# Kernel tuning notes

Measured on AMD Instinct MI355X. Metric: run time of the kernel, lower is better.

The kernel has to match this reference:

```python
import jax, jax.numpy as jnp
import numpy as np

DIM = 64
N_EMBED = 1024
POS_DIM = 16
POS_EMBED = 128


def _build_mask(dim, n_embed, pos_dim, pos_embed):
    # mask[dim-pos_dim:, :n_embed-pos_embed] = 0 ; mask[:dim-pos_dim, n_embed-pos_embed:] = 0
    m = np.ones((dim, n_embed), dtype=np.float32)
    m[dim - pos_dim:, : n_embed - pos_embed] = 0.0
    m[: dim - pos_dim, n_embed - pos_embed:] = 0.0
    return jnp.asarray(m)


def setup_inputs() -> dict:
    key = jax.random.key(0)
    k1, k2 = jax.random.split(key)
    inp = jax.random.normal(k1, (64, 32, 32, DIM), dtype=jnp.float32)  # [B,H,W,dim]
    embed = jax.random.normal(k2, (DIM, N_EMBED), dtype=jnp.float32)   # codebook buffer
    return {"input": inp, "embed": embed, "bi": 1}


def reference(input, embed, bi):
    dim, n_embed = embed.shape
    mask = _build_mask(dim, n_embed, POS_DIM, POS_EMBED)
    embed_m = embed * mask  # self.embed = embed * mask

    # select codebook columns depending on branch
    if bi == 1:
        cols = embed_m                              # [dim, n_embed]
    else:
        cols = embed_m[:, : n_embed - POS_EMBED]    # [dim, n_embed - pos_embed]

    flatten = input.reshape(-1, dim)  # [N, dim]
    # squared euclidean distance: ||f||^2 - 2 f.e + ||e||^2
    dist = (
        jnp.sum(flatten * flatten, axis=1, keepdims=True)
        - 2.0 * flatten @ cols
        + jnp.sum(cols * cols, axis=0, keepdims=True)
    )  # [N, K]
    embed_ind = jnp.argmin(dist, axis=1)                 # argmax of -dist
    embed_ind = embed_ind.reshape(input.shape[:-1])      # [B,H,W]

    # embedding lookup: F.embedding(ind, cols.T)
    quantize = jnp.take(cols.T, embed_ind, axis=0)       # [B,H,W,dim]

    diff = jnp.mean(
        (jax.lax.stop_gradient(quantize) - input) ** 2, axis=(1, 2, 3)
    )  # [B]
    quantize_st = input + jax.lax.stop_gradient(quantize - input)  # straight-through
    return (quantize_st, diff, embed_ind, embed_m)
```

## Files before the change

kernel.cpp:

```cpp
#include <hip/hip_runtime.h>

#define N_ROWS 65536
#define DIM    64
#define NE     1024
#define NPOS   128
#define KSPLIT 48

#define OFF_DIFF  (N_ROWS * DIM)
#define OFF_IND   (OFF_DIFF + 64)
#define OFF_EMBM  (OFF_IND + N_ROWS)


__global__ __launch_bounds__(64) void k_prep(const float* __restrict__ embed,
                                             float* __restrict__ out,
                                             float* __restrict__ colsT,
                                             float* __restrict__ cnh) {
    int c = blockIdx.x * 64 + threadIdx.x;
    bool clow = c < (NE - NPOS);
    float s = 0.f;
#pragma unroll
    for (int j = 0; j < DIM / 4; ++j) {
        float v0 = embed[(4 * j + 0) * NE + c];
        float v1 = embed[(4 * j + 1) * NE + c];
        float v2 = embed[(4 * j + 2) * NE + c];
        float v3 = embed[(4 * j + 3) * NE + c];
        v0 = (((4 * j + 0) < KSPLIT) == clow) ? v0 : 0.f;
        v1 = (((4 * j + 1) < KSPLIT) == clow) ? v1 : 0.f;
        v2 = (((4 * j + 2) < KSPLIT) == clow) ? v2 : 0.f;
        v3 = (((4 * j + 3) < KSPLIT) == clow) ? v3 : 0.f;
        out[OFF_EMBM + (4 * j + 0) * NE + c] = v0;
        out[OFF_EMBM + (4 * j + 1) * NE + c] = v1;
        out[OFF_EMBM + (4 * j + 2) * NE + c] = v2;
        out[OFF_EMBM + (4 * j + 3) * NE + c] = v3;
        colsT[c * DIM + 4 * j + 0] = v0;
        colsT[c * DIM + 4 * j + 1] = v1;
        colsT[c * DIM + 4 * j + 2] = v2;
        colsT[c * DIM + 4 * j + 3] = v3;
        s += v0 * v0 + v1 * v1 + v2 * v2 + v3 * v3;
    }
    cnh[c] = 0.5f * s;
    if (c < 64) out[OFF_DIFF + c] = 0.f;
}

#define FMA4(XJ, V) { a0 += XJ.x * V.x; a1 += XJ.y * V.y; a2 += XJ.z * V.z; a3 += XJ.w * V.w; }

#define DOT_A(C, OUT) { \
    const float4* __restrict__ p4 = (const float4*)(colsT + (C) * DIM); \
    float a0 = 0.f, a1 = 0.f, a2 = 0.f, a3 = 0.f; float4 v; \
    v = p4[0];  FMA4(x0,  v); \
    v = p4[1];  FMA4(x1,  v); \
    v = p4[2];  FMA4(x2,  v); \
    v = p4[3];  FMA4(x3,  v); \
    v = p4[4];  FMA4(x4,  v); \
    v = p4[5];  FMA4(x5,  v); \
    v = p4[6];  FMA4(x6,  v); \
    v = p4[7];  FMA4(x7,  v); \
    v = p4[8];  FMA4(x8,  v); \
    v = p4[9];  FMA4(x9,  v); \
    v = p4[10]; FMA4(x10, v); \
    v = p4[11]; FMA4(x11, v); \
    OUT = (a0 + a1) + (a2 + a3); }

#define DOT_B(C, OUT) { \
    const float4* __restrict__ p4 = (const float4*)(colsT + (C) * DIM); \
    float a0 = 0.f, a1 = 0.f, a2 = 0.f, a3 = 0.f; float4 v; \
    v = p4[12]; FMA4(x12, v); \
    v = p4[13]; FMA4(x13, v); \
    v = p4[14]; FMA4(x14, v); \
    v = p4[15]; FMA4(x15, v); \
    OUT = (a0 + a1) + (a2 + a3); }

#define TAKE(SC, C) { float a_ = (SC) - cnh[(C)]; bool g_ = a_ > best; \
    best = g_ ? a_ : best; bidx = g_ ? (C) : bidx; }

__global__ __launch_bounds__(512, 8) void k_main(const float* __restrict__ input,
                                                 const float* __restrict__ colsT,
                                                 const float* __restrict__ cnh,
                                                 float* __restrict__ out) {
    const int wave = __builtin_amdgcn_readfirstlane(threadIdx.x >> 6);
    const int lane = threadIdx.x & 63;
    const int row  = blockIdx.x * 64 + lane;

    const float4* __restrict__ xp = (const float4*)(input + (size_t)row * DIM);
    float4 x0  = xp[0],  x1  = xp[1],  x2  = xp[2],  x3  = xp[3];
    float4 x4  = xp[4],  x5  = xp[5],  x6  = xp[6],  x7  = xp[7];
    float4 x8  = xp[8],  x9  = xp[9],  x10 = xp[10], x11 = xp[11];
    float4 x12 = xp[12], x13 = xp[13], x14 = xp[14], x15 = xp[15];

    float best = -3.0e38f;
    int   bidx = 0;

    const int cbeg = wave * 112;
    for (int c0 = cbeg; c0 < cbeg + 112; c0 += 4) {
        float s0, s1, s2, s3;
        DOT_A(c0 + 0, s0);
        DOT_A(c0 + 1, s1);
        DOT_A(c0 + 2, s2);
        DOT_A(c0 + 3, s3);
        TAKE(s0, c0 + 0);
        TAKE(s1, c0 + 1);
        TAKE(s2, c0 + 2);
        TAKE(s3, c0 + 3);
    }

    const int dbeg = (NE - NPOS) + wave * 16;
    for (int c0 = dbeg; c0 < dbeg + 16; c0 += 4) {
        float s0, s1, s2, s3;
        DOT_B(c0 + 0, s0);
        DOT_B(c0 + 1, s1);
        DOT_B(c0 + 2, s2);
        DOT_B(c0 + 3, s3);
        TAKE(s0, c0 + 0);
        TAKE(s1, c0 + 1);
        TAKE(s2, c0 + 2);
        TAKE(s3, c0 + 3);
    }

    __shared__ float sbest[8][64];
    __shared__ int   sidx[8][64];
    sbest[wave][lane] = best;
    sidx[wave][lane]  = bidx;
    __syncthreads();

    if (wave == 0) {
        float b  = sbest[0][lane];
        int   bi = sidx[0][lane];
#pragma unroll
        for (int w = 1; w < 8; ++w) {
            float bw = sbest[w][lane];
            int   iw = sidx[w][lane];
            bool g = (bw > b) || (bw == b && iw < bi);
            b  = g ? bw : b;
            bi = g ? iw : bi;
        }

        const float4* __restrict__ qp = (const float4*)(colsT + bi * DIM);
        float4* __restrict__ oq = (float4*)(out + (size_t)row * DIM);
        float s = 0.f;
#define EPI(J, XJ) { float4 q = qp[J]; \
        float d0 = q.x - XJ.x, d1 = q.y - XJ.y, d2 = q.z - XJ.z, d3 = q.w - XJ.w; \
        float4 r; r.x = XJ.x + d0; r.y = XJ.y + d1; r.z = XJ.z + d2; r.w = XJ.w + d3; \
        oq[J] = r; s += d0 * d0 + d1 * d1 + d2 * d2 + d3 * d3; }
        EPI(0,  x0);  EPI(1,  x1);  EPI(2,  x2);  EPI(3,  x3);
        EPI(4,  x4);  EPI(5,  x5);  EPI(6,  x6);  EPI(7,  x7);
        EPI(8,  x8);  EPI(9,  x9);  EPI(10, x10); EPI(11, x11);
        EPI(12, x12); EPI(13, x13); EPI(14, x14); EPI(15, x15);
#undef EPI

        out[OFF_IND + row] = (float)bi;

#pragma unroll
        for (int off = 32; off > 0; off >>= 1)
            s += __shfl_down(s, off, 64);
        if (lane == 0)
            atomicAdd(out + OFF_DIFF + (blockIdx.x >> 4),
                      s * (1.0f / (32.0f * 32.0f * 64.0f)));
    }
}

extern "C" void kernel_launch(void* const* d_in, const int* in_sizes, int n_in,
                              void* d_out, int out_size, void* d_ws, size_t ws_size,
                              hipStream_t stream) {
    const float* input = (const float*)d_in[0];
    const float* embed = (const float*)d_in[1];

    float* out   = (float*)d_out;
    float* colsT = (float*)d_ws;
    float* cnh   = colsT + NE * DIM;

    k_prep<<<16, 64, 0, stream>>>(embed, out, colsT, cnh);
    k_main<<<1024, 512, 0, stream>>>(input, colsT, cnh, out);
}
```

Before: 213.5 us.

## Stage codebook chunks in per-wave LDS and use 4 waves per block

Each wave now copies 32-column chunks of the transposed codebook into its own LDS slice with coalesced loads, then reads them as broadcast LDS loads instead of uniform global loads. The block shrinks from 8 to 4 waves, so each wave scans 224+32 columns and the final cross-wave reduction covers 4 entries. This aims to cut global/L1 traffic per dot product, at the cost of LDS usage, fewer waves in flight for hiding latency, and a wave-local write-then-read in LDS with no explicit barrier.

```diff
diff --git a/kernel.cpp b/kernel.cpp
--- a/kernel.cpp
+++ b/kernel.cpp
@@ -44,42 +44,44 @@
 
 #define FMA4(XJ, V) { a0 += XJ.x * V.x; a1 += XJ.y * V.y; a2 += XJ.z * V.z; a3 += XJ.w * V.w; }
 
-#define DOT_A(C, OUT) { \
-    const float4* __restrict__ p4 = (const float4*)(colsT + (C) * DIM); \
+#define DOT_A_LDS(CP, OUT) { \
     float a0 = 0.f, a1 = 0.f, a2 = 0.f, a3 = 0.f; float4 v; \
-    v = p4[0];  FMA4(x0,  v); \
-    v = p4[1];  FMA4(x1,  v); \
-    v = p4[2];  FMA4(x2,  v); \
-    v = p4[3];  FMA4(x3,  v); \
-    v = p4[4];  FMA4(x4,  v); \
-    v = p4[5];  FMA4(x5,  v); \
-    v = p4[6];  FMA4(x6,  v); \
-    v = p4[7];  FMA4(x7,  v); \
-    v = p4[8];  FMA4(x8,  v); \
-    v = p4[9];  FMA4(x9,  v); \
-    v = p4[10]; FMA4(x10, v); \
-    v = p4[11]; FMA4(x11, v); \
+    v = CP[0];  FMA4(x0,  v); \
+    v = CP[1];  FMA4(x1,  v); \
+    v = CP[2];  FMA4(x2,  v); \
+    v = CP[3];  FMA4(x3,  v); \
+    v = CP[4];  FMA4(x4,  v); \
+    v = CP[5];  FMA4(x5,  v); \
+    v = CP[6];  FMA4(x6,  v); \
+    v = CP[7];  FMA4(x7,  v); \
+    v = CP[8];  FMA4(x8,  v); \
+    v = CP[9];  FMA4(x9,  v); \
+    v = CP[10]; FMA4(x10, v); \
+    v = CP[11]; FMA4(x11, v); \
     OUT = (a0 + a1) + (a2 + a3); }
 
-#define DOT_B(C, OUT) { \
-    const float4* __restrict__ p4 = (const float4*)(colsT + (C) * DIM); \
+#define DOT_B_LDS(CP, OUT) { \
     float a0 = 0.f, a1 = 0.f, a2 = 0.f, a3 = 0.f; float4 v; \
-    v = p4[12]; FMA4(x12, v); \
-    v = p4[13]; FMA4(x13, v); \
-    v = p4[14]; FMA4(x14, v); \
-    v = p4[15]; FMA4(x15, v); \
+    v = CP[12]; FMA4(x12, v); \
+    v = CP[13]; FMA4(x13, v); \
+    v = CP[14]; FMA4(x14, v); \
+    v = CP[15]; FMA4(x15, v); \
     OUT = (a0 + a1) + (a2 + a3); }
 
 #define TAKE(SC, C) { float a_ = (SC) - cnh[(C)]; bool g_ = a_ > best; \
     best = g_ ? a_ : best; bidx = g_ ? (C) : bidx; }
 
-__global__ __launch_bounds__(512, 8) void k_main(const float* __restrict__ input,
+__global__ __launch_bounds__(256, 4) void k_main(const float* __restrict__ input,
                                                  const float* __restrict__ colsT,
                                                  const float* __restrict__ cnh,
                                                  float* __restrict__ out) {
     const int wave = __builtin_amdgcn_readfirstlane(threadIdx.x >> 6);
     const int lane = threadIdx.x & 63;
     const int row  = blockIdx.x * 64 + lane;
+
+    __shared__ float4 lds4[4 * 32 * 16];
+    __shared__ float  sbest[4][64];
+    __shared__ int    sidx[4][64];
 
     const float4* __restrict__ xp = (const float4*)(input + (size_t)row * DIM);
     float4 x0  = xp[0],  x1  = xp[1],  x2  = xp[2],  x3  = xp[3];
@@ -90,34 +92,55 @@
     float best = -3.0e38f;
     int   bidx = 0;
 
-    const int cbeg = wave * 112;
-    for (int c0 = cbeg; c0 < cbeg + 112; c0 += 4) {
-        float s0, s1, s2, s3;
-        DOT_A(c0 + 0, s0);
-        DOT_A(c0 + 1, s1);
-        DOT_A(c0 + 2, s2);
-        DOT_A(c0 + 3, s3);
-        TAKE(s0, c0 + 0);
-        TAKE(s1, c0 + 1);
-        TAKE(s2, c0 + 2);
-        TAKE(s3, c0 + 3);
+    const float4* __restrict__ colsT4 = (const float4*)colsT;
+    float4* __restrict__ ldst = lds4 + wave * 512;
+
+    for (int i = 0; i < 7; ++i) {
+        const int cb = 224 * wave + 32 * i;
+#pragma unroll
+        for (int t = 0; t < 8; ++t)
+            ldst[t * 64 + lane] = colsT4[(size_t)cb * 16 + t * 64 + lane];
+#pragma unroll 2
+        for (int j = 0; j < 32; j += 4) {
+            const float4* __restrict__ cp0 = ldst + (j + 0) * 16;
+            const float4* __restrict__ cp1 = ldst + (j + 1) * 16;
+            const float4* __restrict__ cp2 = ldst + (j + 2) * 16;
+            const float4* __restrict__ cp3 = ldst + (j + 3) * 16;
+            float s0, s1, s2, s3;
+            DOT_A_LDS(cp0, s0);
+            DOT_A_LDS(cp1, s1);
+            DOT_A_LDS(cp2, s2);
+            DOT_A_LDS(cp3, s3);
+            TAKE(s0, cb + j + 0);
+            TAKE(s1, cb + j + 1);
+            TAKE(s2, cb + j + 2);
+            TAKE(s3, cb + j + 3);
+        }
     }
 
-    const int dbeg = (NE - NPOS) + wave * 16;
-    for (int c0 = dbeg; c0 < dbeg + 16; c0 += 4) {
-        float s0, s1, s2, s3;
-        DOT_B(c0 + 0, s0);
-        DOT_B(c0 + 1, s1);
-        DOT_B(c0 + 2, s2);
-        DOT_B(c0 + 3, s3);
-        TAKE(s0, c0 + 0);
-        TAKE(s1, c0 + 1);
-        TAKE(s2, c0 + 2);
-        TAKE(s3, c0 + 3);
+    {
+        const int cb = (NE - NPOS) + 32 * wave;
+#pragma unroll
+        for (int t = 0; t < 8; ++t)
+            ldst[t * 64 + lane] = colsT4[(size_t)cb * 16 + t * 64 + lane];
+#pragma unroll 2
+        for (int j = 0; j < 32; j += 4) {
+            const float4* __restrict__ cp0 = ldst + (j + 0) * 16;
+            const float4* __restrict__ cp1 = ldst + (j + 1) * 16;
+            const float4* __restrict__ cp2 = ldst + (j + 2) * 16;
+            const float4* __restrict__ cp3 = ldst + (j + 3) * 16;
+            float s0, s1, s2, s3;
+            DOT_B_LDS(cp0, s0);
+            DOT_B_LDS(cp1, s1);
+            DOT_B_LDS(cp2, s2);
+            DOT_B_LDS(cp3, s3);
+            TAKE(s0, cb + j + 0);
+            TAKE(s1, cb + j + 1);
+            TAKE(s2, cb + j + 2);
+            TAKE(s3, cb + j + 3);
+        }
     }
 
-    __shared__ float sbest[8][64];
-    __shared__ int   sidx[8][64];
     sbest[wave][lane] = best;
     sidx[wave][lane]  = bidx;
     __syncthreads();
@@ -126,7 +149,7 @@
         float b  = sbest[0][lane];
         int   bi = sidx[0][lane];
 #pragma unroll
-        for (int w = 1; w < 8; ++w) {
+        for (int w = 1; w < 4; ++w) {
             float bw = sbest[w][lane];
             int   iw = sidx[w][lane];
             bool g = (bw > b) || (bw == b && iw < bi);
@@ -169,5 +192,5 @@
     float* cnh   = colsT + NE * DIM;
 
     k_prep<<<16, 64, 0, stream>>>(embed, out, colsT, cnh);
-    k_main<<<1024, 512, 0, stream>>>(input, colsT, cnh, out);
+    k_main<<<1024, 256, 0, stream>>>(input, colsT, cnh, out);
 }
```

New measurement: 215.9 us. Within noise of the previous version (+1.1%).
